# Optimization experiments

Measured on AMD Instinct MI355X. Metric: run time of the kernel, lower is better.

Reference implementation:

```python
import jax, jax.numpy as jnp
import numpy as np

COMMITMENT_COST = 0.25
EPS = 1e-12  # matches torch F.normalize default eps


def _l2norm(v, axis=-1):
    n = jnp.linalg.norm(v, axis=axis, keepdims=True)
    return v / jnp.maximum(n, EPS)


def setup_inputs() -> dict:
    key = jax.random.key(0)
    k1, k2 = jax.random.split(key)
    x = jax.random.normal(k1, (65536, 256), dtype=jnp.float32)
    codebook = jax.random.normal(k2, (4096, 256), dtype=jnp.float32)
    return {"x": x, "codebook": codebook}


def reference(x, codebook):
    # x: [N, D] latents; codebook: [K, D] embedding table
    xn = _l2norm(x)                 # [N, D]
    cbn = _l2norm(codebook)         # [K, D]

    # Squared L2 distances: ||xn||^2 + ||cbn||^2 - 2 xn.cbn^T  -> [N, K]
    dists = (
        jnp.sum(xn * xn, axis=-1, keepdims=True)
        + jnp.sum(cbn * cbn, axis=1)
        - 2.0 * jnp.einsum("nd,kd->nk", xn, cbn)
    )
    idx = jnp.argmin(dists, axis=1)  # [N]

    # quantize: gather then L2-normalize (matches F.normalize(embeddings(idx)))
    quantized = _l2norm(cbn[idx])    # [N, D]

    q_latent_loss = jnp.mean((quantized - jax.lax.stop_gradient(xn)) ** 2)
    e_latent_loss = jnp.mean((xn - jax.lax.stop_gradient(quantized)) ** 2)
    loss = q_latent_loss + COMMITMENT_COST * e_latent_loss

    # straight-through estimator
    quantized_st = xn + jax.lax.stop_gradient(quantized - xn)
    return quantized_st, loss, idx
```

## Files before the change

### kernel.cpp

```cpp
#include <hip/hip_runtime.h>
#include <math.h>

#define N_ROWS 65536
#define DIM    256
#define NCODE  4096
#define MARGIN 2e-4f
#define TILE_C 32
#define NTILE  (NCODE / TILE_C)
#define FB     8
#define KCH    1024
#define NCH    (NCODE / KCH)
#define FIXG   512

typedef __attribute__((ext_vector_type(8)))  short short8v;
typedef __attribute__((ext_vector_type(4)))  float float4v;
typedef __attribute__((ext_vector_type(16))) float f32x16;

__device__ inline unsigned short f2bf(float f) {
    unsigned u = __float_as_uint(f);
    unsigned r = (u + 0x7fffu + ((u >> 16) & 1u)) >> 16;
    return (unsigned short)r;
}
__device__ inline float bf2f(unsigned short h) {
    return __uint_as_float(((unsigned)h) << 16);
}
__device__ inline void gll16(const void* g, void* l) {
    __builtin_amdgcn_global_load_lds(
        (const __attribute__((address_space(1))) unsigned int*)g,
        (__attribute__((address_space(3))) unsigned int*)l, 16, 0, 0);
}

__global__ void cb_norm_kernel(const float* __restrict__ cb,
                               unsigned short* __restrict__ pk,
                               float* __restrict__ c2,
                               double* __restrict__ c2d,
                               double* __restrict__ ndi) {
    int k = blockIdx.x;
    int t = threadIdx.x;
    float v = cb[k * DIM + t];
    double dv = (double)v;
    double ss = dv * dv;
    __shared__ double red2[4], red3[4], redn[4];
    #pragma unroll
    for (int off = 32; off > 0; off >>= 1) ss += __shfl_down(ss, off);
    if ((t & 63) == 0) redn[t >> 6] = ss;
    __syncthreads();
    double S = redn[0] + redn[1] + redn[2] + redn[3];
    double nrm = fmax(sqrt(S), 1e-12);
    double cq = dv / nrm;
    float cf = (float)cq;
    unsigned short hb = f2bf(cf);
    unsigned short lb = f2bf(cf - bf2f(hb));
    {
        int cb32 = k >> 5, klo = k & 31, ks = t >> 4, hi = (t >> 3) & 1, j = t & 7;
        size_t ch = ((size_t)cb32 * 16 + ks) * 2;
        size_t slot = (size_t)(hi * 32 + klo) * 8 + j;
        pk[(ch + 0) * 512 + slot] = hb;
        pk[(ch + 1) * 512 + slot] = lb;
    }
    double s2 = (double)cf * (double)cf;
    double s3 = cq * cq;
    #pragma unroll
    for (int off = 32; off > 0; off >>= 1) {
        s2 += __shfl_down(s2, off);
        s3 += __shfl_down(s3, off);
    }
    if ((t & 63) == 0) { red2[t >> 6] = s2; red3[t >> 6] = s3; }
    __syncthreads();
    if (t == 0) {
        c2[k]  = (float)(red2[0] + red2[1] + red2[2] + red2[3]);
        c2d[k] = red3[0] + red3[1] + red3[2] + red3[3];
        ndi[k] = 1.0 / nrm;
    }
}

__global__ void x_norm_kernel(const float* __restrict__ x,
                              float* __restrict__ nx,
                              float* __restrict__ scx,
                              int* __restrict__ counter) {
    if (blockIdx.x == 0 && threadIdx.x == 0) counter[0] = 0;
    int w = threadIdx.x >> 6;
    int lane = threadIdx.x & 63;
    int row = blockIdx.x * 4 + w;
    float4 v = ((const float4*)(x + (size_t)row * DIM))[lane];
    double ss = (double)v.x * v.x + (double)v.y * v.y
              + (double)v.z * v.z + (double)v.w * v.w;
    #pragma unroll
    for (int off = 32; off > 0; off >>= 1) ss += __shfl_down(ss, off);
    if (lane == 0) {
        double n = fmax(sqrt(ss), 1e-12);
        nx[row]  = (float)n;
        scx[row] = (float)(2.0 / n);
    }
}

__attribute__((amdgpu_waves_per_eu(2, 2)))
__global__ void __launch_bounds__(256)
argmin_mfma_kernel(const float* __restrict__ x,
                   const unsigned short* __restrict__ pk,
                   const float* __restrict__ c2,
                   const float* __restrict__ scx,
                   int* __restrict__ idx_out,
                   int* __restrict__ counter,
                   int* __restrict__ rowlist) {
    __shared__ unsigned short buf[2][16384];
    __shared__ float c2s[NCODE];

    int tid  = threadIdx.x;
    int lane = tid & 63;
    int wave = tid >> 6;
    int cl31 = lane & 31;
    int hi   = lane >> 5;
    int xbase = blockIdx.x * 128 + wave * 32;

    #pragma unroll
    for (int i = 0; i < NCODE / 256; i++) c2s[i * 256 + tid] = c2[i * 256 + tid];

    short8v bh[16], bl[16];
    const float* xr = x + (size_t)(xbase + cl31) * DIM + hi * 8;
    #pragma unroll
    for (int ks = 0; ks < 16; ks++) {
        float4 f0 = *(const float4*)(xr + ks * 16);
        float4 f1 = *(const float4*)(xr + ks * 16 + 4);
        float e[8] = {f0.x, f0.y, f0.z, f0.w, f1.x, f1.y, f1.z, f1.w};
        short8v h, l;
        #pragma unroll
        for (int j = 0; j < 8; j++) {
            unsigned short hb = f2bf(e[j]);
            h[j] = (short)hb;
            l[j] = (short)f2bf(e[j] - bf2f(hb));
        }
        bh[ks] = h;
        bl[ks] = l;
    }
    float scr = scx[xbase + cl31];

    float s1 = 3.4e38f, s2 = 3.4e38f;
    int   i1 = 0x7fffffff;

    {
        const unsigned short* src = pk + ((size_t)wave * 8) * 512 + lane * 8;
        unsigned short* dst = &buf[0][(wave * 8) * 512];
        #pragma unroll
        for (int i = 0; i < 8; i++) gll16(src + i * 512, dst + i * 512);
    }
    __syncthreads();

    int cur = 0;
    for (int t = 0; t < NTILE; t++) {
        int cbb = t * TILE_C;

        if (t + 1 < NTILE) {
            const unsigned short* src =
                pk + ((size_t)(t + 1) * 32 + wave * 8) * 512 + lane * 8;
            unsigned short* dst = &buf[cur ^ 1][(wave * 8) * 512];
            #pragma unroll
            for (int i = 0; i < 8; i++) gll16(src + i * 512, dst + i * 512);
        }

        const unsigned short* cbuf = &buf[cur][0];
        f32x16 a1 = {0.f,0.f,0.f,0.f,0.f,0.f,0.f,0.f,0.f,0.f,0.f,0.f,0.f,0.f,0.f,0.f};
        f32x16 a2 = a1, a3 = a1;
        #pragma unroll
        for (int ks = 0; ks < 16; ks++) {
            short8v ah = *(const short8v*)(cbuf + (size_t)(ks * 2 + 0) * 512 + lane * 8);
            short8v al = *(const short8v*)(cbuf + (size_t)(ks * 2 + 1) * 512 + lane * 8);
            a1 = __builtin_amdgcn_mfma_f32_32x32x16_bf16(ah, bh[ks], a1, 0, 0, 0);
            a2 = __builtin_amdgcn_mfma_f32_32x32x16_bf16(ah, bl[ks], a2, 0, 0, 0);
            a3 = __builtin_amdgcn_mfma_f32_32x32x16_bf16(al, bh[ks], a3, 0, 0, 0);
        }

        float4v gq0 = *(const float4v*)&c2s[cbb + hi * 4];
        float4v gq1 = *(const float4v*)&c2s[cbb + hi * 4 + 8];
        float4v gq2 = *(const float4v*)&c2s[cbb + hi * 4 + 16];
        float4v gq3 = *(const float4v*)&c2s[cbb + hi * 4 + 24];
        float sv[16];
        float mn = 3.4e38f;
        #pragma unroll
        for (int g = 0; g < 4; g++) {
            float4v gg = (g == 0) ? gq0 : (g == 1) ? gq1 : (g == 2) ? gq2 : gq3;
            #pragma unroll
            for (int q = 0; q < 4; q++) {
                int r = g * 4 + q;
                float s = gg[q] - scr * (a1[r] + a2[r] + a3[r]);
                sv[r] = s;
                mn = fminf(mn, s);
            }
        }
        if (!__all(mn >= s2)) {
            #pragma unroll
            for (int g = 0; g < 4; g++) {
                #pragma unroll
                for (int q = 0; q < 4; q++) {
                    float s = sv[g * 4 + q];
                    int ci = cbb + q + 8 * g + 4 * hi;
                    if (s < s1) { s2 = s1; s1 = s; i1 = ci; }
                    else if (s < s2) s2 = s;
                }
            }
        }

        __syncthreads();
        cur ^= 1;
    }

    {
        float o1 = __shfl_xor(s1, 32);
        int   oi = __shfl_xor(i1, 32);
        float o2 = __shfl_xor(s2, 32);
        if (o1 < s1 || (o1 == s1 && oi < i1)) { s2 = fminf(s1, o2); s1 = o1; i1 = oi; }
        else                                   { s2 = fminf(o1, s2); }
    }
    if (lane < 32) {
        int row = xbase + lane;
        idx_out[row] = i1;
        if (s2 - s1 < MARGIN) { int slot = atomicAdd(counter, 1); rowlist[slot] = row; }
    }
}

__global__ void fixup2d_kernel(const float* __restrict__ x,
                               const float* __restrict__ cb,
                               const double* __restrict__ c2d,
                               const double* __restrict__ ndi,
                               const int* __restrict__ counter,
                               const int* __restrict__ rowlist,
                               double* __restrict__ pb_s,
                               int* __restrict__ pb_i) {
    __shared__ double xs[FB][DIM];
    __shared__ double isx_sh[FB];
    __shared__ double red_s[4][FB];
    __shared__ int    red_i[4][FB];
    int t = threadIdx.x, lane = t & 63, wave = t >> 6;
    int cnt = counter[0];
    int nbat = (cnt + FB - 1) / FB;
    int nwork = nbat * NCH;

    for (int w = blockIdx.x; w < nwork; w += FIXG) {
        int batch = w / NCH, chunk = w - batch * NCH;
        int base = batch * FB;
        int nb = cnt - base; if (nb > FB) nb = FB;

        #pragma unroll
        for (int r = 0; r < FB; r++)
            if (r < nb) xs[r][t] = (double)x[(size_t)rowlist[base + r] * DIM + t];
        __syncthreads();

        for (int rr = wave; rr < nb; rr += 4) {
            double a0 = xs[rr][lane],       a1 = xs[rr][lane + 64];
            double a2 = xs[rr][lane + 128], a3 = xs[rr][lane + 192];
            double ss = a0 * a0 + a1 * a1 + a2 * a2 + a3 * a3;
            #pragma unroll
            for (int m = 1; m < 64; m <<= 1) ss += __shfl_xor(ss, m);
            if (lane == 0) isx_sh[rr] = 2.0 / fmax(sqrt(ss), 1e-12);
        }
        __syncthreads();

        double bs[FB]; int bi[FB];
        #pragma unroll
        for (int r = 0; r < FB; r++) { bs[r] = 1e300; bi[r] = 0x7fffffff; }

        for (int k0 = 0; k0 < KCH / 256; k0++) {
            int k = chunk * KCH + k0 * 256 + t;
            const float4* cr = (const float4*)(cb + (size_t)k * DIM);
            double d[FB];
            #pragma unroll
            for (int r = 0; r < FB; r++) d[r] = 0.0;
            #pragma unroll 4
            for (int d4 = 0; d4 < DIM / 4; d4++) {
                float4 c = cr[d4];
                double cx = c.x, cy = c.y, cz = c.z, cw = c.w;
                int dd = d4 * 4;
                #pragma unroll
                for (int r = 0; r < FB; r++) {
                    d[r] = fma(cx, xs[r][dd],     d[r]);
                    d[r] = fma(cy, xs[r][dd + 1], d[r]);
                    d[r] = fma(cz, xs[r][dd + 2], d[r]);
                    d[r] = fma(cw, xs[r][dd + 3], d[r]);
                }
            }
            double ndik = ndi[k], c2k = c2d[k];
            #pragma unroll
            for (int r = 0; r < FB; r++) {
                double sc = c2k - isx_sh[r] * d[r] * ndik;
                if (sc < bs[r] || (sc == bs[r] && k < bi[r])) { bs[r] = sc; bi[r] = k; }
            }
        }

        #pragma unroll
        for (int r = 0; r < FB; r++) {
            double b = bs[r]; int idx = bi[r];
            #pragma unroll
            for (int m = 1; m < 64; m <<= 1) {
                double ob = __shfl_xor(b, m);
                int   oi = __shfl_xor(idx, m);
                if (ob < b || (ob == b && oi < idx)) { b = ob; idx = oi; }
            }
            if (lane == 0) { red_s[wave][r] = b; red_i[wave][r] = idx; }
        }
        __syncthreads();
        if (t < nb) {
            double b = red_s[0][t]; int idx = red_i[0][t];
            #pragma unroll
            for (int ww = 1; ww < 4; ww++) {
                double ob = red_s[ww][t]; int oi = red_i[ww][t];
                if (ob < b || (ob == b && oi < idx)) { b = ob; idx = oi; }
            }
            pb_s[(size_t)(base + t) * NCH + chunk] = b;
            pb_i[(size_t)(base + t) * NCH + chunk] = idx;
        }
        __syncthreads();
    }
}

__global__ void fixmerge_kernel(const int* __restrict__ counter,
                                const int* __restrict__ rowlist,
                                const double* __restrict__ pb_s,
                                const int* __restrict__ pb_i,
                                int* __restrict__ idxv) {
    int cnt = counter[0];
    for (int s = blockIdx.x * 256 + threadIdx.x; s < cnt; s += gridDim.x * 256) {
        double b = pb_s[(size_t)s * NCH]; int idx = pb_i[(size_t)s * NCH];
        #pragma unroll
        for (int c = 1; c < NCH; c++) {
            double ob = pb_s[(size_t)s * NCH + c]; int oi = pb_i[(size_t)s * NCH + c];
            if (ob < b || (ob == b && oi < idx)) { b = ob; idx = oi; }
        }
        idxv[rowlist[s]] = idx;
    }
}

__global__ void gather_loss_kernel(const float* __restrict__ x,
                                   const float* __restrict__ cb,
                                   const double* __restrict__ ndi,
                                   const float* __restrict__ nx,
                                   const int* __restrict__ idxv,
                                   float* __restrict__ out_q,
                                   float* __restrict__ out_idxf,
                                   float* __restrict__ partials) {
    int w = threadIdx.x >> 6, lane = threadIdx.x & 63;
    int row = blockIdx.x * 4 + w;
    int iv = idxv[row];
    float ndif = (float)ndi[iv];
    float inx = 1.0f / nx[row];
    float4 q4 = ((const float4*)(cb + (size_t)iv * DIM))[lane];
    float4 x4 = ((const float4*)(x + (size_t)row * DIM))[lane];
    float4 qq;
    qq.x = q4.x * ndif; qq.y = q4.y * ndif;
    qq.z = q4.z * ndif; qq.w = q4.w * ndif;
    ((float4*)(out_q + (size_t)row * DIM))[lane] = qq;
    float dx = qq.x - x4.x * inx;
    float dy = qq.y - x4.y * inx;
    float dz = qq.z - x4.z * inx;
    float dw = qq.w - x4.w * inx;
    float ss = dx * dx + dy * dy + dz * dz + dw * dw;
    #pragma unroll
    for (int off = 32; off > 0; off >>= 1) ss += __shfl_down(ss, off);
    if (lane == 0) {
        partials[row] = ss;
        out_idxf[row] = (float)iv;
    }
}

__global__ void loss_reduce_kernel(const float* __restrict__ partials,
                                   float* __restrict__ out_loss) {
    int t = threadIdx.x;
    float s = 0.0f;
    for (int i = t; i < N_ROWS; i += 256) s += partials[i];
    __shared__ float red[4];
    #pragma unroll
    for (int off = 32; off > 0; off >>= 1) s += __shfl_down(s, off);
    if ((t & 63) == 0) red[t >> 6] = s;
    __syncthreads();
    if (t == 0) out_loss[0] = 1.25f * (red[0] + red[1] + red[2] + red[3]) / (float)(N_ROWS * DIM);
}

extern "C" void kernel_launch(void* const* d_in, const int* in_sizes, int n_in,
                              void* d_out, int out_size, void* d_ws, size_t ws_size,
                              hipStream_t stream) {
    const float* x  = (const float*)d_in[0];
    const float* cb = (const float*)d_in[1];
    float* out = (float*)d_out;

    double* c2d  = (double*)d_ws;
    double* ndi  = c2d + NCODE;
    double* pb_s = ndi + NCODE;
    float*  c2   = (float*)(pb_s + (size_t)N_ROWS * NCH);
    float*  nx   = c2 + NCODE;
    float*  scx  = nx + N_ROWS;
    int*    idxv = (int*)(scx + N_ROWS);
    float*  partials = (float*)(idxv + N_ROWS);
    int*    counter  = (int*)(partials + N_ROWS);
    int*    rowlist  = counter + 8;
    int*    pb_i     = rowlist + N_ROWS;
    unsigned short* pk = (unsigned short*)(pb_i + (size_t)N_ROWS * NCH);

    float* out_q    = out;
    float* out_loss = out + (size_t)N_ROWS * DIM;
    float* out_idxf = out_loss + 1;

    hipLaunchKernelGGL(cb_norm_kernel, dim3(NCODE), dim3(256), 0, stream,
                       cb, pk, c2, c2d, ndi);
    hipLaunchKernelGGL(x_norm_kernel, dim3(N_ROWS / 4), dim3(256), 0, stream, x, nx, scx, counter);
    hipLaunchKernelGGL(argmin_mfma_kernel, dim3(N_ROWS / 128), dim3(256), 0, stream,
                       x, pk, c2, scx, idxv, counter, rowlist);
    hipLaunchKernelGGL(fixup2d_kernel, dim3(FIXG), dim3(256), 0, stream,
                       x, cb, c2d, ndi, counter, rowlist, pb_s, pb_i);
    hipLaunchKernelGGL(fixmerge_kernel, dim3(64), dim3(256), 0, stream,
                       counter, rowlist, pb_s, pb_i, idxv);
    hipLaunchKernelGGL(gather_loss_kernel, dim3(N_ROWS / 4), dim3(256), 0, stream,
                       x, cb, ndi, nx, idxv, out_q, out_idxf, partials);
    hipLaunchKernelGGL(loss_reduce_kernel, dim3(1), dim3(256), 0, stream,
                       partials, out_loss);
}
```

Baseline: 601.4 us.

## Process two 32-row x tiles per wave to reuse codebook LDS reads

Each wave now handles 64 rows instead of 32, so each codebook fragment loaded from LDS feeds six MFMAs covering two row tiles. The three split-precision products per tile now go into one accumulator instead of three. Together these halve the LDS traffic and codebook global loads per row and cut the number of blocks in half. The cost is twice the register footprint for x fragments, which risks spilling at the forced 2 waves/EU, fewer blocks (256) to fill the CUs, and a serial dependency chain on each accumulator.

```diff
diff --git a/kernel.cpp b/kernel.cpp
--- a/kernel.cpp
+++ b/kernel.cpp
@@ -111,32 +111,51 @@
     int wave = tid >> 6;
     int cl31 = lane & 31;
     int hi   = lane >> 5;
-    int xbase = blockIdx.x * 128 + wave * 32;
+    int xbase = blockIdx.x * 256 + wave * 64;
 
     #pragma unroll
     for (int i = 0; i < NCODE / 256; i++) c2s[i * 256 + tid] = c2[i * 256 + tid];
 
-    short8v bh[16], bl[16];
-    const float* xr = x + (size_t)(xbase + cl31) * DIM + hi * 8;
-    #pragma unroll
-    for (int ks = 0; ks < 16; ks++) {
-        float4 f0 = *(const float4*)(xr + ks * 16);
-        float4 f1 = *(const float4*)(xr + ks * 16 + 4);
-        float e[8] = {f0.x, f0.y, f0.z, f0.w, f1.x, f1.y, f1.z, f1.w};
-        short8v h, l;
-        #pragma unroll
-        for (int j = 0; j < 8; j++) {
-            unsigned short hb = f2bf(e[j]);
-            h[j] = (short)hb;
-            l[j] = (short)f2bf(e[j] - bf2f(hb));
-        }
-        bh[ks] = h;
-        bl[ks] = l;
-    }
-    float scr = scx[xbase + cl31];
-
-    float s1 = 3.4e38f, s2 = 3.4e38f;
-    int   i1 = 0x7fffffff;
+    short8v bh0[16], bl0[16], bh1[16], bl1[16];
+    {
+        const float* xr0 = x + (size_t)(xbase + cl31) * DIM + hi * 8;
+        const float* xr1 = x + (size_t)(xbase + 32 + cl31) * DIM + hi * 8;
+        #pragma unroll
+        for (int ks = 0; ks < 16; ks++) {
+            float4 f0 = *(const float4*)(xr0 + ks * 16);
+            float4 f1 = *(const float4*)(xr0 + ks * 16 + 4);
+            float e[8] = {f0.x, f0.y, f0.z, f0.w, f1.x, f1.y, f1.z, f1.w};
+            short8v h, l;
+            #pragma unroll
+            for (int j = 0; j < 8; j++) {
+                unsigned short hb = f2bf(e[j]);
+                h[j] = (short)hb;
+                l[j] = (short)f2bf(e[j] - bf2f(hb));
+            }
+            bh0[ks] = h;
+            bl0[ks] = l;
+        }
+        #pragma unroll
+        for (int ks = 0; ks < 16; ks++) {
+            float4 f0 = *(const float4*)(xr1 + ks * 16);
+            float4 f1 = *(const float4*)(xr1 + ks * 16 + 4);
+            float e[8] = {f0.x, f0.y, f0.z, f0.w, f1.x, f1.y, f1.z, f1.w};
+            short8v h, l;
+            #pragma unroll
+            for (int j = 0; j < 8; j++) {
+                unsigned short hb = f2bf(e[j]);
+                h[j] = (short)hb;
+                l[j] = (short)f2bf(e[j] - bf2f(hb));
+            }
+            bh1[ks] = h;
+            bl1[ks] = l;
+        }
+    }
+    float scr0 = scx[xbase + cl31];
+    float scr1 = scx[xbase + 32 + cl31];
+
+    float s1a = 3.4e38f, s2a = 3.4e38f, s1b = 3.4e38f, s2b = 3.4e38f;
+    int   i1a = 0x7fffffff, i1b = 0x7fffffff;
 
     {
         const unsigned short* src = pk + ((size_t)wave * 8) * 512 + lane * 8;
@@ -159,43 +178,60 @@
         }
 
         const unsigned short* cbuf = &buf[cur][0];
-        f32x16 a1 = {0.f,0.f,0.f,0.f,0.f,0.f,0.f,0.f,0.f,0.f,0.f,0.f,0.f,0.f,0.f,0.f};
-        f32x16 a2 = a1, a3 = a1;
+        f32x16 a0 = {0.f,0.f,0.f,0.f,0.f,0.f,0.f,0.f,0.f,0.f,0.f,0.f,0.f,0.f,0.f,0.f};
+        f32x16 a1 = a0;
         #pragma unroll
         for (int ks = 0; ks < 16; ks++) {
             short8v ah = *(const short8v*)(cbuf + (size_t)(ks * 2 + 0) * 512 + lane * 8);
             short8v al = *(const short8v*)(cbuf + (size_t)(ks * 2 + 1) * 512 + lane * 8);
-            a1 = __builtin_amdgcn_mfma_f32_32x32x16_bf16(ah, bh[ks], a1, 0, 0, 0);
-            a2 = __builtin_amdgcn_mfma_f32_32x32x16_bf16(ah, bl[ks], a2, 0, 0, 0);
-            a3 = __builtin_amdgcn_mfma_f32_32x32x16_bf16(al, bh[ks], a3, 0, 0, 0);
+            a0 = __builtin_amdgcn_mfma_f32_32x32x16_bf16(ah, bh0[ks], a0, 0, 0, 0);
+            a1 = __builtin_amdgcn_mfma_f32_32x32x16_bf16(ah, bh1[ks], a1, 0, 0, 0);
+            a0 = __builtin_amdgcn_mfma_f32_32x32x16_bf16(ah, bl0[ks], a0, 0, 0, 0);
+            a1 = __builtin_amdgcn_mfma_f32_32x32x16_bf16(ah, bl1[ks], a1, 0, 0, 0);
+            a0 = __builtin_amdgcn_mfma_f32_32x32x16_bf16(al, bh0[ks], a0, 0, 0, 0);
+            a1 = __builtin_amdgcn_mfma_f32_32x32x16_bf16(al, bh1[ks], a1, 0, 0, 0);
         }
 
         float4v gq0 = *(const float4v*)&c2s[cbb + hi * 4];
         float4v gq1 = *(const float4v*)&c2s[cbb + hi * 4 + 8];
         float4v gq2 = *(const float4v*)&c2s[cbb + hi * 4 + 16];
         float4v gq3 = *(const float4v*)&c2s[cbb + hi * 4 + 24];
-        float sv[16];
-        float mn = 3.4e38f;
+        float sva[16], svb[16];
+        float mna = 3.4e38f, mnb = 3.4e38f;
         #pragma unroll
         for (int g = 0; g < 4; g++) {
             float4v gg = (g == 0) ? gq0 : (g == 1) ? gq1 : (g == 2) ? gq2 : gq3;
             #pragma unroll
             for (int q = 0; q < 4; q++) {
                 int r = g * 4 + q;
-                float s = gg[q] - scr * (a1[r] + a2[r] + a3[r]);
-                sv[r] = s;
-                mn = fminf(mn, s);
-            }
-        }
-        if (!__all(mn >= s2)) {
+                float sa = gg[q] - scr0 * a0[r];
+                float sb = gg[q] - scr1 * a1[r];
+                sva[r] = sa; svb[r] = sb;
+                mna = fminf(mna, sa);
+                mnb = fminf(mnb, sb);
+            }
+        }
+        if (!__all(mna >= s2a)) {
             #pragma unroll
             for (int g = 0; g < 4; g++) {
                 #pragma unroll
                 for (int q = 0; q < 4; q++) {
-                    float s = sv[g * 4 + q];
+                    float s = sva[g * 4 + q];
                     int ci = cbb + q + 8 * g + 4 * hi;
-                    if (s < s1) { s2 = s1; s1 = s; i1 = ci; }
-                    else if (s < s2) s2 = s;
+                    if (s < s1a) { s2a = s1a; s1a = s; i1a = ci; }
+                    else if (s < s2a) s2a = s;
+                }
+            }
+        }
+        if (!__all(mnb >= s2b)) {
+            #pragma unroll
+            for (int g = 0; g < 4; g++) {
+                #pragma unroll
+                for (int q = 0; q < 4; q++) {
+                    float s = svb[g * 4 + q];
+                    int ci = cbb + q + 8 * g + 4 * hi;
+                    if (s < s1b) { s2b = s1b; s1b = s; i1b = ci; }
+                    else if (s < s2b) s2b = s;
                 }
             }
         }
@@ -205,16 +241,24 @@
     }
 
     {
-        float o1 = __shfl_xor(s1, 32);
-        int   oi = __shfl_xor(i1, 32);
-        float o2 = __shfl_xor(s2, 32);
-        if (o1 < s1 || (o1 == s1 && oi < i1)) { s2 = fminf(s1, o2); s1 = o1; i1 = oi; }
-        else                                   { s2 = fminf(o1, s2); }
+        float o1 = __shfl_xor(s1a, 32);
+        int   oi = __shfl_xor(i1a, 32);
+        float o2 = __shfl_xor(s2a, 32);
+        if (o1 < s1a || (o1 == s1a && oi < i1a)) { s2a = fminf(s1a, o2); s1a = o1; i1a = oi; }
+        else                                      { s2a = fminf(o1, s2a); }
+        o1 = __shfl_xor(s1b, 32);
+        oi = __shfl_xor(i1b, 32);
+        o2 = __shfl_xor(s2b, 32);
+        if (o1 < s1b || (o1 == s1b && oi < i1b)) { s2b = fminf(s1b, o2); s1b = o1; i1b = oi; }
+        else                                      { s2b = fminf(o1, s2b); }
     }
     if (lane < 32) {
         int row = xbase + lane;
-        idx_out[row] = i1;
-        if (s2 - s1 < MARGIN) { int slot = atomicAdd(counter, 1); rowlist[slot] = row; }
+        idx_out[row] = i1a;
+        if (s2a - s1a < MARGIN) { int slot = atomicAdd(counter, 1); rowlist[slot] = row; }
+        row = xbase + 32 + lane;
+        idx_out[row] = i1b;
+        if (s2b - s1b < MARGIN) { int slot = atomicAdd(counter, 1); rowlist[slot] = row; }
     }
 }
 
@@ -401,7 +445,7 @@
     hipLaunchKernelGGL(cb_norm_kernel, dim3(NCODE), dim3(256), 0, stream,
                        cb, pk, c2, c2d, ndi);
     hipLaunchKernelGGL(x_norm_kernel, dim3(N_ROWS / 4), dim3(256), 0, stream, x, nx, scx, counter);
-    hipLaunchKernelGGL(argmin_mfma_kernel, dim3(N_ROWS / 128), dim3(256), 0, stream,
+    hipLaunchKernelGGL(argmin_mfma_kernel, dim3(N_ROWS / 256), dim3(256), 0, stream,
                        x, pk, c2, scx, idxv, counter, rowlist);
     hipLaunchKernelGGL(fixup2d_kernel, dim3(FIXG), dim3(256), 0, stream,
                        x, cb, c2d, ndi, counter, rowlist, pb_s, pb_i);
```

Measured after the change: 1.009 ms. 1.68x slower.
